# Kernel tuning notes

Hardware: AMD Instinct MI355X
Metric: run time of the kernel (lower is better)

The kernel has to match this reference:

```python
import jax, jax.numpy as jnp
import numpy as np

N_NODES = 100000
N_FEAT = 512
HIDDEN = 16
OUT = 2
N_EDGES = 3200000


def gcn_conv(x, edge_index, W, b, n_nodes):
    """PyG-style GCNConv: h = D^-1/2 (A+I) D^-1/2 (x W) + b."""
    h = x @ W  # project first (PyG order) -> [N, out]
    src, dst = edge_index[0], edge_index[1]
    # add self loops
    loop = jnp.arange(n_nodes, dtype=src.dtype)
    src = jnp.concatenate([src, loop])
    dst = jnp.concatenate([dst, loop])
    # symmetric normalization: deg = in-degree (scatter ones to dst)
    deg = jax.ops.segment_sum(jnp.ones_like(dst, dtype=h.dtype), dst, num_segments=n_nodes)
    dinv = jax.lax.rsqrt(deg)  # deg >= 1 due to self loops
    norm = dinv[src] * dinv[dst]  # [E+N]
    msg = h[src] * norm[:, None]  # gather + scale
    out = jax.ops.segment_sum(msg, dst, num_segments=n_nodes)  # scatter-add
    return out + b


def setup_inputs() -> dict:
    key = jax.random.key(0)
    k1, k2, k3, k4, k5 = jax.random.split(key, 5)
    x = jax.random.normal(k1, (N_NODES, N_FEAT), dtype=jnp.float32)
    edge_index = jax.random.randint(k2, (2, N_EDGES), 0, N_NODES, dtype=jnp.int64)
    # Glorot-style params for the two GCNConv layers
    W1 = jax.random.normal(k3, (N_FEAT, HIDDEN), dtype=jnp.float32) / np.sqrt(N_FEAT)
    b1 = jnp.zeros((HIDDEN,), dtype=jnp.float32)
    W2 = jax.random.normal(k4, (HIDDEN, OUT), dtype=jnp.float32) / np.sqrt(HIDDEN)
    b2 = jnp.zeros((OUT,), dtype=jnp.float32)
    return {"x": x, "edge_index": edge_index, "W1": W1, "b1": b1, "W2": W2, "b2": b2}


def reference(x, edge_index, W1, b1, W2, b2):
    n = x.shape[0]
    h = gcn_conv(x, edge_index, W1, b1, n)
    h = jax.nn.relu(h)
    out = gcn_conv(h, edge_index, W2, b2, n)
    return out
```

## Files before the change

kernel.cpp:

```cpp
#include <hip/hip_runtime.h>
#include <hip/hip_fp16.h>

#define NFEAT 512
#define HID 16
#define MAXNB 512
#define NBLK 512
#define PACK_SHIFT 17
#define PACK_MASK ((1 << PACK_SHIFT) - 1)

typedef _Float16 f16x8 __attribute__((ext_vector_type(8)));
typedef float f32x4 __attribute__((ext_vector_type(4)));

__device__ __forceinline__ void gemm_tile(const float* __restrict__ x,
                                          const float* __restrict__ W,
                                          __half* __restrict__ h1u,
                                          int tile, int N, int lane) {
  const int n = lane & 15;
  const int g = lane >> 4;

  f16x8 bf[16];
#pragma unroll
  for (int f = 0; f < 16; ++f) {
    const float* wp = W + (size_t)(f * 32 + g * 8) * HID + n;
#pragma unroll
    for (int j = 0; j < 8; ++j) bf[f][j] = (_Float16)wp[j * HID];
  }

  int rowbase = tile * 16;
  if (rowbase + 16 > N) rowbase = N - 16;
  const float* xr = x + (size_t)(rowbase + n) * NFEAT + g * 8;

  f32x4 acc = {0.f, 0.f, 0.f, 0.f};
#pragma unroll
  for (int f = 0; f < 16; ++f) {
    float4 p0 = *(const float4*)(xr + f * 32);
    float4 p1 = *(const float4*)(xr + f * 32 + 4);
    f16x8 af;
    af[0] = (_Float16)p0.x; af[1] = (_Float16)p0.y;
    af[2] = (_Float16)p0.z; af[3] = (_Float16)p0.w;
    af[4] = (_Float16)p1.x; af[5] = (_Float16)p1.y;
    af[6] = (_Float16)p1.z; af[7] = (_Float16)p1.w;
    acc = __builtin_amdgcn_mfma_f32_16x16x32_f16(af, bf[f], acc, 0, 0, 0);
  }

#pragma unroll
  for (int r = 0; r < 4; ++r) {
    int row = rowbase + g * 4 + r;
    h1u[(size_t)row * HID + n] = __float2half(acc[r]);
  }
}

__global__ __launch_bounds__(512) void k_hist_gemm(const int* __restrict__ ei,
                                                   int* __restrict__ cnt_t,
                                                   int E, int nb,
                                                   const float* __restrict__ x,
                                                   const float* __restrict__ W,
                                                   __half* __restrict__ h1u,
                                                   int N, int tsplit) {
  __shared__ int l[2][MAXNB];
  if (blockIdx.x < NBLK) {
    for (int i = threadIdx.x; i < nb; i += 512) {
      l[0][i] = 0;
      l[1][i] = 0;
    }
    __syncthreads();
    const int par = threadIdx.x & 1;
    int chunk = (E + NBLK - 1) / NBLK;
    int beg = blockIdx.x * chunk;
    int end = beg + chunk; if (end > E) end = E;
    for (int e = beg + threadIdx.x; e < end; e += 512)
      atomicAdd(&l[par][ei[(size_t)E + e] >> 8], 1);
    __syncthreads();
    for (int b = threadIdx.x; b < nb; b += 512)
      cnt_t[(size_t)b * NBLK + blockIdx.x] = l[0][b] + l[1][b];
  } else {
    int tile = (blockIdx.x - NBLK) * 8 + (threadIdx.x >> 6);
    if (tile < tsplit) gemm_tile(x, W, h1u, tile, N, threadIdx.x & 63);
  }
}

__global__ __launch_bounds__(64) void k_colscan(const int* __restrict__ cnt_t,
                                                int* __restrict__ off_t,
                                                int* __restrict__ gcnt, int nb) {
  int b = blockIdx.x;
  if (b >= nb) return;
  int lane = threadIdx.x;
  int4 v0 = *(const int4*)&cnt_t[(size_t)b * NBLK + lane * 8];
  int4 v1 = *(const int4*)&cnt_t[(size_t)b * NBLK + lane * 8 + 4];
  int tot = (v0.x + v0.y + v0.z + v0.w) + (v1.x + v1.y + v1.z + v1.w);
  int s = tot;
  for (int d = 1; d < 64; d <<= 1) {
    int o = __shfl_up(s, d);
    if (lane >= d) s += o;
  }
  int excl = s - tot;
  int4 w0, w1;
  w0.x = excl;
  w0.y = w0.x + v0.x;
  w0.z = w0.y + v0.y;
  w0.w = w0.z + v0.z;
  w1.x = w0.w + v0.w;
  w1.y = w1.x + v1.x;
  w1.z = w1.y + v1.y;
  w1.w = w1.z + v1.z;
  *(int4*)&off_t[(size_t)b * NBLK + lane * 8] = w0;
  *(int4*)&off_t[(size_t)b * NBLK + lane * 8 + 4] = w1;
  if (lane == 63) gcnt[b] = s;
}

__global__ __launch_bounds__(512) void k_bscan(const int* __restrict__ gcnt,
                                               int* __restrict__ gbase, int nb) {
  __shared__ int sm[512];
  int t = threadIdx.x;
  int c = (t < nb) ? gcnt[t] : 0;
  int pc = (c + 15) & ~15;
  sm[t] = pc;
  __syncthreads();
  for (int off = 1; off < 512; off <<= 1) {
    int x = (t >= off) ? sm[t - off] : 0;
    __syncthreads();
    sm[t] += x;
    __syncthreads();
  }
  if (t < nb) gbase[t] = sm[t] - pc;
}

__global__ __launch_bounds__(512) void k_scatter_gemm(const int* __restrict__ ei,
                                                      const int* __restrict__ gbase,
                                                      const int* __restrict__ off_t,
                                                      int* __restrict__ binned,
                                                      int E, int nb,
                                                      const float* __restrict__ x,
                                                      const float* __restrict__ W,
                                                      __half* __restrict__ h1u,
                                                      int N, int tsplit, int ntiles) {
  __shared__ int cur[MAXNB];
  if (blockIdx.x < NBLK) {
    for (int b = threadIdx.x; b < nb; b += 512)
      cur[b] = gbase[b] + off_t[(size_t)b * NBLK + blockIdx.x];
    __syncthreads();
    int chunk = (E + NBLK - 1) / NBLK;
    int beg = blockIdx.x * chunk;
    int end = beg + chunk; if (end > E) end = E;
    for (int e = beg + threadIdx.x; e < end; e += 512) {
      int s = ei[e];
      int d = ei[(size_t)E + e];
      int b = d >> 8;
      int pos = atomicAdd(&cur[b], 1);
      binned[pos] = s | ((d & 255) << PACK_SHIFT);
    }
  } else {
    int tile = tsplit + (blockIdx.x - NBLK) * 8 + (threadIdx.x >> 6);
    if (tile < ntiles) gemm_tile(x, W, h1u, tile, N, threadIdx.x & 63);
  }
}

__global__ __launch_bounds__(512) void k_sortbucket(const int* __restrict__ gbase,
                                                    const int* __restrict__ gcnt,
                                                    const int* __restrict__ binned,
                                                    int* __restrict__ csr,
                                                    int* __restrict__ rowbeg,
                                                    int* __restrict__ rowend,
                                                    float* __restrict__ dinv,
                                                    __half* __restrict__ h1h, int N) {
  __shared__ int hist[2][256];
  __shared__ int sm[256];
  __shared__ int cur[256];
  __shared__ float sdinv[256];
  const int t = threadIdx.x;
  const int b = blockIdx.x;
  const int base = gbase[b], cnt = gcnt[b];
  if (t < 256) {
    hist[0][t] = 0;
    hist[1][t] = 0;
  }
  __syncthreads();
  const int par = t & 1;
  for (int j = base + t; j < base + cnt; j += 512)
    atomicAdd(&hist[par][binned[j] >> PACK_SHIFT], 1);
  __syncthreads();
  int h = 0;
  if (t < 256) {
    h = hist[0][t] + hist[1][t];
    sm[t] = h;
  }
  __syncthreads();
  for (int off = 1; off < 256; off <<= 1) {
    int x = 0;
    if (t < 256 && t >= off) x = sm[t - off];
    __syncthreads();
    if (t < 256) sm[t] += x;
    __syncthreads();
  }
  if (t < 256) {
    int incl = sm[t];
    int excl = incl - h;
    cur[t] = excl;
    float dv = rsqrtf((float)h + 1.0f);
    sdinv[t] = dv;
    int node = b * 256 + t;
    if (node < N) {
      rowbeg[node] = base + excl;
      rowend[node] = base + incl;
      dinv[node] = dv;
    }
  }
  __syncthreads();
  for (int j = base + t; j < base + cnt; j += 512) {
    int val = binned[j];
    int pos = atomicAdd(&cur[val >> PACK_SHIFT], 1);
    csr[base + pos] = val & PACK_MASK;
  }
  {
    int node = b * 256 + (t >> 1);
    if (node < N) {
      float dv = sdinv[t >> 1];
      __half* hp = h1h + (size_t)node * HID + (t & 1) * 8;
      f16x8 v = *(const f16x8*)hp;
#pragma unroll
      for (int j = 0; j < 8; ++j) v[j] = (_Float16)((float)v[j] * dv);
      *(f16x8*)hp = v;
    }
  }
}

__global__ __launch_bounds__(256) void k_agg1f(const int* __restrict__ rowbeg,
                                               const int* __restrict__ rowend,
                                               const int* __restrict__ csr,
                                               const __half* __restrict__ h1h,
                                               const float* __restrict__ dinv,
                                               const float* __restrict__ b1,
                                               const float* __restrict__ W2,
                                               float* __restrict__ h2s, int N) {
  const int f = threadIdx.x & 15;
  const int node = blockIdx.x * 16 + (threadIdx.x >> 4);
  if (node >= N) return;
  int j = rowbeg[node];
  const int end = rowend[node];
  float acc = __half2float(h1h[(size_t)node * HID + f]);
  for (; j < end && (j & 3); ++j) acc += __half2float(h1h[(size_t)csr[j] * HID + f]);
  for (; j + 8 <= end; j += 8) {
    int4 s0 = *(const int4*)&csr[j];
    int4 s1 = *(const int4*)&csr[j + 4];
    float a0 = __half2float(h1h[(size_t)s0.x * HID + f]);
    float a1 = __half2float(h1h[(size_t)s0.y * HID + f]);
    float a2 = __half2float(h1h[(size_t)s0.z * HID + f]);
    float a3 = __half2float(h1h[(size_t)s0.w * HID + f]);
    float a4 = __half2float(h1h[(size_t)s1.x * HID + f]);
    float a5 = __half2float(h1h[(size_t)s1.y * HID + f]);
    float a6 = __half2float(h1h[(size_t)s1.z * HID + f]);
    float a7 = __half2float(h1h[(size_t)s1.w * HID + f]);
    acc += ((a0 + a1) + (a2 + a3)) + ((a4 + a5) + (a6 + a7));
  }
  for (; j + 4 <= end; j += 4) {
    int4 ss = *(const int4*)&csr[j];
    float a0 = __half2float(h1h[(size_t)ss.x * HID + f]);
    float a1 = __half2float(h1h[(size_t)ss.y * HID + f]);
    float a2 = __half2float(h1h[(size_t)ss.z * HID + f]);
    float a3 = __half2float(h1h[(size_t)ss.w * HID + f]);
    acc += (a0 + a1) + (a2 + a3);
  }
  for (; j < end; ++j) acc += __half2float(h1h[(size_t)csr[j] * HID + f]);

  float di = dinv[node];
  float v = fmaxf(acc * di + b1[f], 0.f);
  float o0 = v * W2[f * 2 + 0];
  float o1 = v * W2[f * 2 + 1];
#pragma unroll
  for (int d = 1; d < 16; d <<= 1) {
    o0 += __shfl_xor(o0, d);
    o1 += __shfl_xor(o1, d);
  }
  if (f == 0) *(float2*)&h2s[(size_t)node * 2] = make_float2(o0 * di, o1 * di);
}

__global__ __launch_bounds__(256) void k_agg2f(const int* __restrict__ rowbeg,
                                               const int* __restrict__ rowend,
                                               const int* __restrict__ csr,
                                               const float* __restrict__ h2s,
                                               const float* __restrict__ dinv,
                                               const float* __restrict__ b2,
                                               float* __restrict__ out, int N) {
  const int l = threadIdx.x & 3;
  const int node = blockIdx.x * 64 + (threadIdx.x >> 2);
  if (node >= N) return;
  const int beg = rowbeg[node];
  const int end = rowend[node];
  float ox = 0.f, oy = 0.f;
  for (int j = beg + l; j < end; j += 4) {
    int s = csr[j];
    float2 v = *(const float2*)&h2s[(size_t)s * 2];
    ox += v.x;
    oy += v.y;
  }
  ox += __shfl_xor(ox, 1); oy += __shfl_xor(oy, 1);
  ox += __shfl_xor(ox, 2); oy += __shfl_xor(oy, 2);
  if (l == 0) {
    float2 self = *(const float2*)&h2s[(size_t)node * 2];
    float di = dinv[node];
    float2 o;
    o.x = (ox + self.x) * di + b2[0];
    o.y = (oy + self.y) * di + b2[1];
    *(float2*)&out[(size_t)node * 2] = o;
  }
}

extern "C" void kernel_launch(void* const* d_in, const int* in_sizes, int n_in,
                              void* d_out, int out_size, void* d_ws, size_t ws_size,
                              hipStream_t stream) {
  const float* x = (const float*)d_in[0];
  const int* ei = (const int*)d_in[1];
  const float* W1 = (const float*)d_in[2];
  const float* b1 = (const float*)d_in[3];
  const float* W2 = (const float*)d_in[4];
  const float* b2 = (const float*)d_in[5];
  float* out = (float*)d_out;
  const int N = in_sizes[0] / NFEAT;
  const int E = in_sizes[1] / 2;
  const int nb = (N + 255) / 256;

  char* p = (char*)d_ws;
  int* cnt_t = (int*)p;    p += (size_t)MAXNB * NBLK * 4;
  int* off_t = (int*)p;    p += (size_t)MAXNB * NBLK * 4;
  int* gcnt = (int*)p;     p += (size_t)MAXNB * 4;
  int* gbase = (int*)p;    p += (size_t)MAXNB * 4;
  int* binned = (int*)p;   p += ((size_t)E + MAXNB * 16) * 4;
  int* csr = (int*)p;      p += ((size_t)E + MAXNB * 16) * 4;
  int* rowbeg = (int*)p;   p += (size_t)N * 4;
  int* rowend = (int*)p;   p += (size_t)N * 4;
  float* dinv = (float*)p; p += (size_t)N * 4;
  __half* h1h = (__half*)p; p += (size_t)N * HID * 2;
  float* h2s = (float*)p;  p += (size_t)N * 2 * 4;

  const int ntiles = (N + 15) / 16;
  const int tsplit = ((ntiles / 2) + 7) & ~7;
  const int gA = (tsplit + 7) / 8;
  const int gB = (ntiles - tsplit + 7) / 8;

  k_hist_gemm<<<NBLK + gA, 512, 0, stream>>>(ei, cnt_t, E, nb, x, W1, h1h, N, tsplit);
  k_colscan<<<nb, 64, 0, stream>>>(cnt_t, off_t, gcnt, nb);
  k_bscan<<<1, 512, 0, stream>>>(gcnt, gbase, nb);
  k_scatter_gemm<<<NBLK + gB, 512, 0, stream>>>(ei, gbase, off_t, binned, E, nb,
                                                x, W1, h1h, N, tsplit, ntiles);
  k_sortbucket<<<nb, 512, 0, stream>>>(gbase, gcnt, binned, csr, rowbeg, rowend,
                                       dinv, h1h, N);
  k_agg1f<<<(N + 15) / 16, 256, 0, stream>>>(rowbeg, rowend, csr, h1h, dinv, b1, W2, h2s, N);
  k_agg2f<<<(N + 63) / 64, 256, 0, stream>>>(rowbeg, rowend, csr, h2s, dinv, b2, out, N);
}
```

Before: 166.3 us.

## Drop dual LDS histograms, widen bucket sort block, vectorize agg1 gather to half2

The edge histogram and the bucket-sort histogram each drop the parity-split pair of LDS counters and use a single array. The bucket sort now launches 1024 threads per block. The first aggregation kernel gives each node 8 lanes that each load a half2, so one node's 16-feature row is fetched with half as many lanes and each wave covers twice as many nodes. Single histograms raise LDS atomic contention, and the larger block may reduce occupancy, in exchange for fewer instructions and wider gather loads.

```diff
diff --git a/kernel.cpp b/kernel.cpp
--- a/kernel.cpp
+++ b/kernel.cpp
@@ -57,22 +57,18 @@
                                                    const float* __restrict__ W,
                                                    __half* __restrict__ h1u,
                                                    int N, int tsplit) {
-  __shared__ int l[2][MAXNB];
+  __shared__ int l[MAXNB];
   if (blockIdx.x < NBLK) {
-    for (int i = threadIdx.x; i < nb; i += 512) {
-      l[0][i] = 0;
-      l[1][i] = 0;
-    }
-    __syncthreads();
-    const int par = threadIdx.x & 1;
+    for (int i = threadIdx.x; i < nb; i += 512) l[i] = 0;
+    __syncthreads();
     int chunk = (E + NBLK - 1) / NBLK;
     int beg = blockIdx.x * chunk;
     int end = beg + chunk; if (end > E) end = E;
     for (int e = beg + threadIdx.x; e < end; e += 512)
-      atomicAdd(&l[par][ei[(size_t)E + e] >> 8], 1);
+      atomicAdd(&l[ei[(size_t)E + e] >> 8], 1);
     __syncthreads();
     for (int b = threadIdx.x; b < nb; b += 512)
-      cnt_t[(size_t)b * NBLK + blockIdx.x] = l[0][b] + l[1][b];
+      cnt_t[(size_t)b * NBLK + blockIdx.x] = l[b];
   } else {
     int tile = (blockIdx.x - NBLK) * 8 + (threadIdx.x >> 6);
     if (tile < tsplit) gemm_tile(x, W, h1u, tile, N, threadIdx.x & 63);
@@ -155,33 +151,29 @@
   }
 }
 
-__global__ __launch_bounds__(512) void k_sortbucket(const int* __restrict__ gbase,
-                                                    const int* __restrict__ gcnt,
-                                                    const int* __restrict__ binned,
-                                                    int* __restrict__ csr,
-                                                    int* __restrict__ rowbeg,
-                                                    int* __restrict__ rowend,
-                                                    float* __restrict__ dinv,
-                                                    __half* __restrict__ h1h, int N) {
-  __shared__ int hist[2][256];
+__global__ __launch_bounds__(1024) void k_sortbucket(const int* __restrict__ gbase,
+                                                     const int* __restrict__ gcnt,
+                                                     const int* __restrict__ binned,
+                                                     int* __restrict__ csr,
+                                                     int* __restrict__ rowbeg,
+                                                     int* __restrict__ rowend,
+                                                     float* __restrict__ dinv,
+                                                     __half* __restrict__ h1h, int N) {
+  __shared__ int hist[256];
   __shared__ int sm[256];
   __shared__ int cur[256];
   __shared__ float sdinv[256];
   const int t = threadIdx.x;
   const int b = blockIdx.x;
   const int base = gbase[b], cnt = gcnt[b];
-  if (t < 256) {
-    hist[0][t] = 0;
-    hist[1][t] = 0;
-  }
-  __syncthreads();
-  const int par = t & 1;
-  for (int j = base + t; j < base + cnt; j += 512)
-    atomicAdd(&hist[par][binned[j] >> PACK_SHIFT], 1);
+  if (t < 256) hist[t] = 0;
+  __syncthreads();
+  for (int j = base + t; j < base + cnt; j += 1024)
+    atomicAdd(&hist[binned[j] >> PACK_SHIFT], 1);
   __syncthreads();
   int h = 0;
   if (t < 256) {
-    h = hist[0][t] + hist[1][t];
+    h = hist[t];
     sm[t] = h;
   }
   __syncthreads();
@@ -206,12 +198,12 @@
     }
   }
   __syncthreads();
-  for (int j = base + t; j < base + cnt; j += 512) {
+  for (int j = base + t; j < base + cnt; j += 1024) {
     int val = binned[j];
     int pos = atomicAdd(&cur[val >> PACK_SHIFT], 1);
     csr[base + pos] = val & PACK_MASK;
   }
-  {
+  if (t < 512) {
     int node = b * 256 + (t >> 1);
     if (node < N) {
       float dv = sdinv[t >> 1];
@@ -232,46 +224,58 @@
                                                const float* __restrict__ b1,
                                                const float* __restrict__ W2,
                                                float* __restrict__ h2s, int N) {
-  const int f = threadIdx.x & 15;
-  const int node = blockIdx.x * 16 + (threadIdx.x >> 4);
+  const int l = threadIdx.x & 7;
+  const int node = blockIdx.x * 32 + (threadIdx.x >> 3);
   if (node >= N) return;
+  const __half2* hp = (const __half2*)h1h;
   int j = rowbeg[node];
   const int end = rowend[node];
-  float acc = __half2float(h1h[(size_t)node * HID + f]);
-  for (; j < end && (j & 3); ++j) acc += __half2float(h1h[(size_t)csr[j] * HID + f]);
+  float2 a = __half22float2(hp[(size_t)node * 8 + l]);
+  float accx = a.x, accy = a.y;
+  for (; j < end && (j & 3); ++j) {
+    float2 v = __half22float2(hp[(size_t)csr[j] * 8 + l]);
+    accx += v.x; accy += v.y;
+  }
   for (; j + 8 <= end; j += 8) {
     int4 s0 = *(const int4*)&csr[j];
     int4 s1 = *(const int4*)&csr[j + 4];
-    float a0 = __half2float(h1h[(size_t)s0.x * HID + f]);
-    float a1 = __half2float(h1h[(size_t)s0.y * HID + f]);
-    float a2 = __half2float(h1h[(size_t)s0.z * HID + f]);
-    float a3 = __half2float(h1h[(size_t)s0.w * HID + f]);
-    float a4 = __half2float(h1h[(size_t)s1.x * HID + f]);
-    float a5 = __half2float(h1h[(size_t)s1.y * HID + f]);
-    float a6 = __half2float(h1h[(size_t)s1.z * HID + f]);
-    float a7 = __half2float(h1h[(size_t)s1.w * HID + f]);
-    acc += ((a0 + a1) + (a2 + a3)) + ((a4 + a5) + (a6 + a7));
+    float2 v0 = __half22float2(hp[(size_t)s0.x * 8 + l]);
+    float2 v1 = __half22float2(hp[(size_t)s0.y * 8 + l]);
+    float2 v2 = __half22float2(hp[(size_t)s0.z * 8 + l]);
+    float2 v3 = __half22float2(hp[(size_t)s0.w * 8 + l]);
+    float2 v4 = __half22float2(hp[(size_t)s1.x * 8 + l]);
+    float2 v5 = __half22float2(hp[(size_t)s1.y * 8 + l]);
+    float2 v6 = __half22float2(hp[(size_t)s1.z * 8 + l]);
+    float2 v7 = __half22float2(hp[(size_t)s1.w * 8 + l]);
+    accx += ((v0.x + v1.x) + (v2.x + v3.x)) + ((v4.x + v5.x) + (v6.x + v7.x));
+    accy += ((v0.y + v1.y) + (v2.y + v3.y)) + ((v4.y + v5.y) + (v6.y + v7.y));
   }
   for (; j + 4 <= end; j += 4) {
     int4 ss = *(const int4*)&csr[j];
-    float a0 = __half2float(h1h[(size_t)ss.x * HID + f]);
-    float a1 = __half2float(h1h[(size_t)ss.y * HID + f]);
-    float a2 = __half2float(h1h[(size_t)ss.z * HID + f]);
-    float a3 = __half2float(h1h[(size_t)ss.w * HID + f]);
-    acc += (a0 + a1) + (a2 + a3);
-  }
-  for (; j < end; ++j) acc += __half2float(h1h[(size_t)csr[j] * HID + f]);
-
-  float di = dinv[node];
-  float v = fmaxf(acc * di + b1[f], 0.f);
-  float o0 = v * W2[f * 2 + 0];
-  float o1 = v * W2[f * 2 + 1];
-#pragma unroll
-  for (int d = 1; d < 16; d <<= 1) {
+    float2 v0 = __half22float2(hp[(size_t)ss.x * 8 + l]);
+    float2 v1 = __half22float2(hp[(size_t)ss.y * 8 + l]);
+    float2 v2 = __half22float2(hp[(size_t)ss.z * 8 + l]);
+    float2 v3 = __half22float2(hp[(size_t)ss.w * 8 + l]);
+    accx += (v0.x + v1.x) + (v2.x + v3.x);
+    accy += (v0.y + v1.y) + (v2.y + v3.y);
+  }
+  for (; j < end; ++j) {
+    float2 v = __half22float2(hp[(size_t)csr[j] * 8 + l]);
+    accx += v.x; accy += v.y;
+  }
+
+  const float di = dinv[node];
+  const int f0 = 2 * l;
+  float w0 = fmaxf(accx * di + b1[f0], 0.f);
+  float w1 = fmaxf(accy * di + b1[f0 + 1], 0.f);
+  float o0 = w0 * W2[f0 * 2 + 0] + w1 * W2[(f0 + 1) * 2 + 0];
+  float o1 = w0 * W2[f0 * 2 + 1] + w1 * W2[(f0 + 1) * 2 + 1];
+#pragma unroll
+  for (int d = 1; d < 8; d <<= 1) {
     o0 += __shfl_xor(o0, d);
     o1 += __shfl_xor(o1, d);
   }
-  if (f == 0) *(float2*)&h2s[(size_t)node * 2] = make_float2(o0 * di, o1 * di);
+  if (l == 0) *(float2*)&h2s[(size_t)node * 2] = make_float2(o0 * di, o1 * di);
 }
 
 __global__ __launch_bounds__(256) void k_agg2f(const int* __restrict__ rowbeg,
@@ -342,8 +346,8 @@
   k_bscan<<<1, 512, 0, stream>>>(gcnt, gbase, nb);
   k_scatter_gemm<<<NBLK + gB, 512, 0, stream>>>(ei, gbase, off_t, binned, E, nb,
                                                 x, W1, h1h, N, tsplit, ntiles);
-  k_sortbucket<<<nb, 512, 0, stream>>>(gbase, gcnt, binned, csr, rowbeg, rowend,
-                                       dinv, h1h, N);
-  k_agg1f<<<(N + 15) / 16, 256, 0, stream>>>(rowbeg, rowend, csr, h1h, dinv, b1, W2, h2s, N);
+  k_sortbucket<<<nb, 1024, 0, stream>>>(gbase, gcnt, binned, csr, rowbeg, rowend,
+                                        dinv, h1h, N);
+  k_agg1f<<<(N + 31) / 32, 256, 0, stream>>>(rowbeg, rowend, csr, h1h, dinv, b1, W2, h2s, N);
   k_agg2f<<<(N + 63) / 64, 256, 0, stream>>>(rowbeg, rowend, csr, h2s, dinv, b2, out, N);
 }
```

Result: no change. 164.8 us (median of 2 runs) (-0.9%).
